# Kernel tuning notes

Measured on AMD Instinct MI355X. Metric: run time of the kernel, lower is better.

## Reference

```python
import jax, jax.numpy as jnp
import numpy as np

N_E = 100000   # codebook size (hard-coded 50000/50000 split in source)
E = 768        # e_dim
BETA = 0.25
K = 10         # top-k in source
BUF = 300000   # codebook_used buffer length
SPLIT = 768
B = 512


def _l2n(x):
    # F.normalize(p=2, dim=-1): x / max(||x||, eps)
    return x / jnp.maximum(jnp.linalg.norm(x, axis=-1, keepdims=True), 1e-12)


def _dist(x, y):
    return (x * x).sum(1, keepdims=True) + (y * y).sum(1) - 2.0 * (x @ y.T)


def _quantize(z_flat, cb_norm):
    z_norm = _l2n(z_flat)
    d = _dist(z_norm, cb_norm)
    neg_vals, idx = jax.lax.top_k(-d, K)          # smallest distances, ascending
    w = jax.nn.softmax(neg_vals, axis=1)          # softmax(-distance)
    z_q = jnp.einsum('bk,bkd->bd', w, cb_norm[idx])
    vq = jnp.mean((z_q - jax.lax.stop_gradient(z_flat)) ** 2)
    commit = BETA * jnp.mean((jax.lax.stop_gradient(z_q) - z_flat) ** 2)
    z_q_ste = z_flat + jax.lax.stop_gradient(z_q - z_flat)   # straight-through
    return z_q_ste, vq, commit, idx


def _usage(buf, idx):
    # rolling FIFO buffer of recent code indices; usage = #unique / n_e
    flat = idx.reshape(-1).astype(buf.dtype)
    L = flat.shape[0]
    buf = jnp.concatenate([buf[L:], flat])
    used = jnp.zeros((N_E,), jnp.int32).at[buf].set(1).sum() / N_E
    return buf, used


def setup_inputs() -> dict:
    key = jax.random.key(0)
    ks = jax.random.split(key, 12)
    inp = {
        'z': jax.random.normal(ks[0], (B, 2 * SPLIT), jnp.float32),
        'text_features': jax.random.normal(ks[1], (B, E), jnp.float32),
        'graph_node_features': jax.random.normal(ks[2], (B, E), jnp.float32),
        'batch': B,
        'codebook': jax.random.normal(ks[3], (N_E, E), jnp.float32),
        # MultiheadAttention value/out projections (q/k projs have no effect for seq_len=1)
        'Wv': jax.random.normal(ks[4], (E, E), jnp.float32) * 0.02,
        'bv': jnp.zeros((E,), jnp.float32),
        'Wo': jax.random.normal(ks[5], (E, E), jnp.float32) * 0.02,
        'bo': jnp.zeros((E,), jnp.float32),
        'Wpt': jax.random.normal(ks[6], (E, SPLIT), jnp.float32) * 0.02,
        'bpt': jnp.zeros((E,), jnp.float32),
        'Wpg': jax.random.normal(ks[7], (E, SPLIT), jnp.float32) * 0.02,
        'bpg': jnp.zeros((E,), jnp.float32),
        'codebook_used': jnp.zeros((BUF,), jnp.int32),
    }
    return inp


def reference(z, text_features, graph_node_features, batch, codebook,
              Wv, bv, Wo, bo, Wpt, bpt, Wpg, bpg, codebook_used):
    # --- get_shared_info ---
    # cross_attn with query/key/value all of seq_len 1: softmax over a single key
    # is exactly 1, so output == out_proj(v_proj(value)); eval mode (no dropout).
    vproj = lambda x: x @ Wv.T + bv
    oproj = lambda x: x @ Wo.T + bo
    z_flat_text = oproj(vproj(graph_node_features))   # query=text, value=graph
    z_flat_graph = oproj(vproj(text_features))         # query=graph, value=text

    cb_norm = _l2n(codebook)
    zq_t, vq_t, cm_t, idx_t = _quantize(z_flat_text, cb_norm)
    zq_g, vq_g, cm_g, idx_g = _quantize(z_flat_graph, cb_norm)
    shared_vq = vq_t + vq_g
    shared_commit = cm_t + cm_g
    buf, shared_usage = _usage(codebook_used, jnp.concatenate([idx_t, idx_g], axis=-1))

    # shared_embedding split back into text/graph halves
    shared_text_embedding, shared_graph_embedding = zq_t, zq_g

    # --- specific embeddings ---
    z_text_embedding = z[:, :SPLIT]
    z_graph_embedding = z[:, SPLIT:]
    pt = z_text_embedding @ Wpt.T + bpt
    pg = z_graph_embedding @ Wpg.T + bpg
    cb_text_norm = _l2n(codebook[:50000])
    cb_graph_norm = _l2n(codebook[-50000:])

    sq_t, svq_t, scm_t, sidx_t = _quantize(pt, cb_text_norm)
    buf, text_usage = _usage(buf, sidx_t)
    sq_g, svq_g, scm_g, sidx_g = _quantize(pg, cb_graph_norm)
    buf, graph_usage = _usage(buf, sidx_g)

    return (z_graph_embedding, z_text_embedding,
            shared_text_embedding, shared_graph_embedding,
            shared_vq, shared_commit,
            sq_t, svq_t, scm_t,
            sq_g, svq_g, scm_g,
            shared_usage, text_usage, graph_usage)
```

## Files before the change

### kernel.cpp

```cpp
#include <hip/hip_runtime.h>
#include <hip/hip_bf16.h>

typedef __attribute__((ext_vector_type(8))) short bf16x8;
typedef __attribute__((ext_vector_type(4))) short short4v;
typedef __attribute__((ext_vector_type(4))) float f32x4;

#define NE_      100000
#define EDIM     768
#define HALFCB   50000
#define CHK      1024
#define NCH      49
#define NQT      12
#define QS       1536
#define KTOP     10

#define RN_OFF   0ULL
#define Q_OFF    401408ULL
#define Y_OFF    3547136ULL
#define ZF_OFF   6692864ULL
#define PT_OFF   9838592ULL
#define PG_OFF   11411456ULL
#define CAND_OFF 12984320ULL
#define APP_OFF  25026560ULL
#define FLAG_OFF 25108480ULL
#define CNT_OFF  26308480ULL
#define ACC_OFF  26308544ULL
#define WS_NEED  26308608ULL

#define O_ZQT    786432u
#define O_ZQG    1179648u
#define O_SVQ    1572864u
#define O_SQT    1572866u
#define O_SVQT   1966082u
#define O_SQG    1966084u
#define O_SVQG   2359300u
#define O_USE    2359302u

__device__ __forceinline__ short f2bf(float f) {
  union { float f; unsigned u; } v; v.f = f;
  unsigned r = v.u + 0x7FFFu + ((v.u >> 16) & 1u);
  return (short)(r >> 16);
}

__device__ __forceinline__ void ins10(float v, int idx, float s[10], int id[10]) {
  if (v <= s[0]) return;
  #pragma unroll
  for (int j = 0; j < 10; ++j) {
    bool shift = (j < 9) && (v > s[j + 1]);
    float ns = shift ? s[j + 1] : v;
    int   ni = shift ? id[j + 1] : idx;
    bool upd = shift || (v > s[j]);
    s[j]  = upd ? ns : s[j];
    id[j] = upd ? ni : id[j];
  }
}

__global__ __launch_bounds__(256) void k_rnorm(const float* __restrict__ cb, float* __restrict__ rn) {
  int row = blockIdx.x * 4 + (threadIdx.x >> 6);
  int lane = threadIdx.x & 63;
  const float4* p = (const float4*)(cb + (size_t)row * EDIM);
  float ss = 0.f;
  #pragma unroll
  for (int j = 0; j < 3; ++j) {
    float4 v = p[j * 64 + lane];
    ss += v.x * v.x + v.y * v.y + v.z * v.z + v.w * v.w;
  }
  #pragma unroll
  for (int off = 32; off; off >>= 1) ss += __shfl_xor(ss, off);
  if (lane == 0) rn[row] = 1.0f / fmaxf(sqrtf(ss), 1e-12f);
}

__global__ __launch_bounds__(256) void k_copyz(const float* __restrict__ z, float* __restrict__ out) {
  int i = blockIdx.x * 256 + threadIdx.x;
  int r = i / 192, c = i - r * 192;
  const float4* zr = (const float4*)z + (size_t)r * 384;
  float4 t = zr[c];
  float4 g = zr[192 + c];
  ((float4*)out)[i] = g;
  ((float4*)(out + 393216))[i] = t;
}

__global__ __launch_bounds__(256, 2) void k_gemm_proj(
    const float* __restrict__ A, int lda, const float* __restrict__ W,
    const float* __restrict__ bias, float* __restrict__ C) {
  __shared__ short As[128][72];
  __shared__ short Bs[128][72];
  int tid = threadIdx.x;
  int wave = tid >> 6, lane = tid & 63;
  int wr = wave >> 1, wc = wave & 1;
  int r16 = lane & 15, g8 = (lane >> 4) * 8;
  int m0 = blockIdx.x * 128, n0 = blockIdx.y * 128;
  f32x4 acc[4][4];
  f32x4 zv = {0.f, 0.f, 0.f, 0.f};
  #pragma unroll
  for (int m = 0; m < 4; ++m)
    #pragma unroll
    for (int n = 0; n < 4; ++n) acc[m][n] = zv;

  for (int ks = 0; ks < 12; ++ks) {
    float4 av[8], wv[8];
    #pragma unroll
    for (int i = 0; i < 8; ++i) {
      int id = i * 256 + tid;
      int r = id >> 4, c4 = id & 15;
      av[i] = *((const float4*)(A + (size_t)(m0 + r) * lda + ks * 64) + c4);
      wv[i] = *((const float4*)(W + (size_t)(n0 + r) * EDIM + ks * 64) + c4);
    }
    __syncthreads();
    #pragma unroll
    for (int i = 0; i < 8; ++i) {
      int id = i * 256 + tid;
      int r = id >> 4, c4 = id & 15;
      short4v sa = { f2bf(av[i].x), f2bf(av[i].y), f2bf(av[i].z), f2bf(av[i].w) };
      short4v sw = { f2bf(wv[i].x), f2bf(wv[i].y), f2bf(wv[i].z), f2bf(wv[i].w) };
      *(short4v*)&As[r][c4 * 4] = sa;
      *(short4v*)&Bs[r][c4 * 4] = sw;
    }
    __syncthreads();
    #pragma unroll
    for (int kk = 0; kk < 64; kk += 32) {
      bf16x8 a[4], b[4];
      #pragma unroll
      for (int m = 0; m < 4; ++m) a[m] = *(const bf16x8*)&As[wr * 64 + m * 16 + r16][kk + g8];
      #pragma unroll
      for (int n = 0; n < 4; ++n) b[n] = *(const bf16x8*)&Bs[wc * 64 + n * 16 + r16][kk + g8];
      #pragma unroll
      for (int m = 0; m < 4; ++m)
        #pragma unroll
        for (int n = 0; n < 4; ++n)
          acc[m][n] = __builtin_amdgcn_mfma_f32_16x16x32_bf16(a[m], b[n], acc[m][n], 0, 0, 0);
    }
  }
  #pragma unroll
  for (int n = 0; n < 4; ++n) {
    int col = n0 + wc * 64 + n * 16 + r16;
    float bb = bias[col];
    #pragma unroll
    for (int m = 0; m < 4; ++m) {
      int row = m0 + wr * 64 + m * 16 + (lane >> 4) * 4;
      #pragma unroll
      for (int j = 0; j < 4; ++j)
        C[(size_t)(row + j) * EDIM + col] = acc[m][n][j] + bb;
    }
  }
}

__global__ __launch_bounds__(256) void k_normq(
    const float* __restrict__ ZF, const float* __restrict__ PT,
    const float* __restrict__ PG, short* __restrict__ Q) {
  int row = blockIdx.x * 4 + (threadIdx.x >> 6);
  int lane = threadIdx.x & 63;
  const float* src = (row < 1024) ? ZF + (size_t)row * EDIM
                   : (row < 1536) ? PT + (size_t)(row - 1024) * EDIM
                                  : PG + (size_t)(row - 1536) * EDIM;
  const float4* p = (const float4*)src;
  float4 v[3];
  float ss = 0.f;
  #pragma unroll
  for (int j = 0; j < 3; ++j) {
    v[j] = p[j * 64 + lane];
    ss += v[j].x * v[j].x + v[j].y * v[j].y + v[j].z * v[j].z + v[j].w * v[j].w;
  }
  #pragma unroll
  for (int off = 32; off; off >>= 1) ss += __shfl_xor(ss, off);
  float r = 1.0f / fmaxf(sqrtf(ss), 1e-12f);
  #pragma unroll
  for (int j = 0; j < 3; ++j) {
    short4v s = { f2bf(v[j].x * r), f2bf(v[j].y * r), f2bf(v[j].z * r), f2bf(v[j].w * r) };
    *(short4v*)(Q + (size_t)row * EDIM + (size_t)(j * 64 + lane) * 4) = s;
  }
}

__global__ __launch_bounds__(256, 2) void k_scores(
    const float* __restrict__ cb, const float* __restrict__ rn,
    const short* __restrict__ Q, float2* __restrict__ cand) {
  __shared__ short As[128][72];
  __shared__ short Bs[128][72];
  __shared__ float Sc[128][65];
  int qt = blockIdx.x, ck = blockIdx.y, hh = blockIdx.z;
  int tid = threadIdx.x;
  int wave = tid >> 6, lane = tid & 63;
  int wr = wave >> 1, wc = wave & 1;
  int r16 = lane & 15, g8 = (lane >> 4) * 8;
  int row0 = ck * CHK;
  int nvalid = min(CHK, HALFCB - row0);
  int grow0 = hh * HALFCB + row0;
  int hmax = hh * HALFCB + HALFCB - 1;
  int qbase = qt * 128;
  int q = tid & 127, seg = tid >> 7;

  float s10[10]; int id10[10];
  #pragma unroll
  for (int k = 0; k < 10; ++k) { s10[k] = -3.4e38f; id10[k] = 0; }

  for (int mt = 0; mt < 8; ++mt) {
    f32x4 acc[4][4];
    f32x4 zv = {0.f, 0.f, 0.f, 0.f};
    #pragma unroll
    for (int m = 0; m < 4; ++m)
      #pragma unroll
      for (int n = 0; n < 4; ++n) acc[m][n] = zv;

    for (int ks = 0; ks < 12; ++ks) {
      float4 av[8]; float rsv[8]; uint4 qv[4];
      #pragma unroll
      for (int i = 0; i < 8; ++i) {
        int id = i * 256 + tid;
        int r = id >> 4, c4 = id & 15;
        int gr = grow0 + mt * 128 + r;
        gr = min(gr, hmax);
        av[i] = *((const float4*)(cb + (size_t)gr * EDIM + ks * 64) + c4);
        rsv[i] = rn[gr];
      }
      #pragma unroll
      for (int i = 0; i < 4; ++i) {
        int id = i * 256 + tid;
        int s = id >> 3, c8 = id & 7;
        int slot = qbase + s;
        int qr = (hh && slot >= 1024) ? slot + 512 : slot;
        qv[i] = *((const uint4*)(Q + (size_t)qr * EDIM + ks * 64) + c8);
      }
      __syncthreads();
      #pragma unroll
      for (int i = 0; i < 8; ++i) {
        int id = i * 256 + tid;
        int r = id >> 4, c4 = id & 15;
        short4v sa = { f2bf(av[i].x * rsv[i]), f2bf(av[i].y * rsv[i]),
                       f2bf(av[i].z * rsv[i]), f2bf(av[i].w * rsv[i]) };
        *(short4v*)&As[r][c4 * 4] = sa;
      }
      #pragma unroll
      for (int i = 0; i < 4; ++i) {
        int id = i * 256 + tid;
        int s = id >> 3, c8 = id & 7;
        *(uint4*)&Bs[s][c8 * 8] = qv[i];
      }
      __syncthreads();
      #pragma unroll
      for (int kk = 0; kk < 64; kk += 32) {
        bf16x8 a[4], b[4];
        #pragma unroll
        for (int m = 0; m < 4; ++m) a[m] = *(const bf16x8*)&As[wr * 64 + m * 16 + r16][kk + g8];
        #pragma unroll
        for (int n = 0; n < 4; ++n) b[n] = *(const bf16x8*)&Bs[wc * 64 + n * 16 + r16][kk + g8];
        #pragma unroll
        for (int m = 0; m < 4; ++m)
          #pragma unroll
          for (int n = 0; n < 4; ++n)
            acc[m][n] = __builtin_amdgcn_mfma_f32_16x16x32_bf16(a[m], b[n], acc[m][n], 0, 0, 0);
      }
    }
    #pragma unroll
    for (int p = 0; p < 2; ++p) {
      __syncthreads();
      if (wr == p) {
        #pragma unroll
        for (int n = 0; n < 4; ++n) {
          int c = wc * 64 + n * 16 + r16;
          #pragma unroll
          for (int m = 0; m < 4; ++m) {
            int rl = m * 16 + (lane >> 4) * 4;
            #pragma unroll
            for (int j = 0; j < 4; ++j) Sc[c][rl + j] = acc[m][n][j];
          }
        }
      }
      __syncthreads();
      int rbase = mt * 128 + p * 64 + seg * 32;
      #pragma unroll 4
      for (int j = 0; j < 32; ++j) {
        int rr = rbase + j;
        float v = Sc[q][seg * 32 + j];
        if (rr < nvalid) ins10(v, grow0 + rr, s10, id10);
      }
    }
  }
  __syncthreads();
  float* scf = &Sc[0][0];
  #pragma unroll
  for (int k = 0; k < 10; ++k) {
    scf[tid * 20 + k] = s10[k];
    scf[tid * 20 + 10 + k] = __int_as_float(id10[k]);
  }
  __syncthreads();
  if (tid < 128) {
    int pb = (tid + 128) * 20;
    #pragma unroll
    for (int k = 0; k < 10; ++k) {
      float v = scf[pb + k];
      int ip = __float_as_int(scf[pb + 10 + k]);
      ins10(v, ip, s10, id10);
    }
    float2* cp = cand + ((size_t)(hh * QS + qbase + tid) * NCH + ck) * KTOP;
    #pragma unroll
    for (int k = 0; k < 10; ++k) cp[k] = make_float2(s10[k], __int_as_float(id10[k]));
  }
}

__global__ __launch_bounds__(256) void k_topk(
    const float2* __restrict__ cand, const float* __restrict__ cb,
    const float* __restrict__ rn, const float* __restrict__ ZF,
    const float* __restrict__ PT, const float* __restrict__ PG,
    float* __restrict__ out, int* __restrict__ app, float* __restrict__ accs) {
  int wave = threadIdx.x >> 6, lane = threadIdx.x & 63;
  int lq = blockIdx.x * 4 + wave;
  int g = lq >> 9, i = lq & 511;
  int slotA = (g == 0) ? i : (g == 1) ? 512 + i : 1024 + i;
  int halfA = (g == 3) ? 1 : 0;
  int n = (g <= 1) ? 980 : 490;
  const float2* baseA = cand + (size_t)(halfA * QS + slotA) * NCH * KTOP;
  const float2* baseB = cand + (size_t)(QS + slotA) * NCH * KTOP;

  float v[16]; int idv[16];
  #pragma unroll
  for (int j = 0; j < 16; ++j) {
    int c = lane + 64 * j;
    float2 e = make_float2(-3.4e38f, 0.f);
    if (c < n) e = (c < 490) ? baseA[c] : baseB[c - 490];
    v[j] = e.x; idv[j] = __float_as_int(e.y);
  }
  unsigned mask = 0xFFFFu;
  float s10[10]; int id10[10];
  #pragma unroll
  for (int r = 0; r < 10; ++r) {
    float bv = -3.4e38f; int bcb = 0x7fffffff; int bpk = 0;
    #pragma unroll
    for (int j = 0; j < 16; ++j) {
      bool alive = (mask >> j) & 1u;
      float vv = alive ? v[j] : -3.4e38f;
      bool take = (vv > bv) || (alive && vv == bv && idv[j] < bcb);
      if (take) { bv = vv; bcb = idv[j]; bpk = (lane << 5) | j; }
    }
    #pragma unroll
    for (int off = 1; off < 64; off <<= 1) {
      float ov = __shfl_xor(bv, off);
      int ocb = __shfl_xor(bcb, off);
      int opk = __shfl_xor(bpk, off);
      bool take = (ov > bv) || (ov == bv && ocb < bcb);
      if (take) { bv = ov; bcb = ocb; bpk = opk; }
    }
    s10[r] = bv; id10[r] = bcb;
    if ((bpk >> 5) == lane) mask &= ~(1u << (bpk & 31u));
  }
  float smax = s10[0];
  float w[10], wsum = 0.f, rnv[10];
  #pragma unroll
  for (int r = 0; r < 10; ++r) { w[r] = expf(2.0f * (s10[r] - smax)); wsum += w[r]; }
  float inv = 1.0f / wsum;
  #pragma unroll
  for (int r = 0; r < 10; ++r) { w[r] *= inv; rnv[r] = rn[id10[r]]; }

  const float* zrow = (g == 0) ? ZF + (size_t)i * EDIM
                    : (g == 1) ? ZF + (size_t)(512 + i) * EDIM
                    : (g == 2) ? PT + (size_t)i * EDIM
                               : PG + (size_t)i * EDIM;
  size_t obase = (size_t)((g == 0) ? O_ZQT : (g == 1) ? O_ZQG : (g == 2) ? O_SQT : O_SQG)
               + (size_t)i * EDIM;
  float vsum = 0.f;
  #pragma unroll
  for (int j = 0; j < 12; ++j) {
    int d = lane + 64 * j;
    float zq = 0.f;
    #pragma unroll
    for (int r = 0; r < 10; ++r) zq += w[r] * cb[(size_t)id10[r] * EDIM + d] * rnv[r];
    out[obase + d] = zq;
    float df = zq - zrow[d];
    vsum += df * df;
  }
  #pragma unroll
  for (int off = 32; off; off >>= 1) vsum += __shfl_xor(vsum, off);
  if (lane == 0) atomicAdd(&accs[g], vsum);
  if (lane < 10) {
    int val = id10[lane];
    if (g == 0)      app[i * 20 + lane] = val;
    else if (g == 1) app[i * 20 + 10 + lane] = val;
    else if (g == 2) app[10240 + i * 10 + lane] = val;
    else             app[15360 + i * 10 + lane] = val - 50000;
  }
}

__global__ __launch_bounds__(256) void k_scatter(
    const int* __restrict__ buf0, const int* __restrict__ app, int* __restrict__ flags) {
  int id = blockIdx.x * 256 + threadIdx.x;
  if (id >= 900000) return;
  int vvar = id / 300000;
  int j = id - vvar * 300000;
  int off = 10240 + 5120 * vvar;
  int keep = 300000 - off;
  int val = (j < keep) ? buf0[off + j] : app[j - keep];
  if (val >= 0 && val < NE_) flags[vvar * NE_ + val] = 1;
}

__global__ __launch_bounds__(256) void k_count(const int* __restrict__ flags, int* __restrict__ cnt) {
  int vvar = blockIdx.y;
  int base = blockIdx.x * 1024;
  int s = 0;
  for (int j = threadIdx.x; j < 1024; j += 256) {
    int idx = base + j;
    if (idx < NE_) s += flags[vvar * NE_ + idx];
  }
  #pragma unroll
  for (int off = 32; off; off >>= 1) s += __shfl_xor(s, off);
  __shared__ int ls[4];
  if ((threadIdx.x & 63) == 0) ls[threadIdx.x >> 6] = s;
  __syncthreads();
  if (threadIdx.x == 0) atomicAdd(&cnt[vvar], ls[0] + ls[1] + ls[2] + ls[3]);
}

__global__ void k_fin(const float* __restrict__ accs, const int* __restrict__ cnt,
                      float* __restrict__ out) {
  if (threadIdx.x == 0) {
    const float inv = 1.0f / (512.0f * 768.0f);
    float vt = accs[0] * inv, vg = accs[1] * inv;
    float vpt = accs[2] * inv, vpg = accs[3] * inv;
    out[O_SVQ]      = vt + vg;
    out[O_SVQ + 1]  = 0.25f * (vt + vg);
    out[O_SVQT]     = vpt;
    out[O_SVQT + 1] = 0.25f * vpt;
    out[O_SVQG]     = vpg;
    out[O_SVQG + 1] = 0.25f * vpg;
    out[O_USE]      = (float)cnt[0] / 100000.0f;
    out[O_USE + 1]  = (float)cnt[1] / 100000.0f;
    out[O_USE + 2]  = (float)cnt[2] / 100000.0f;
  }
}

extern "C" void kernel_launch(void* const* d_in, const int* in_sizes, int n_in,
                              void* d_out, int out_size, void* d_ws, size_t ws_size,
                              hipStream_t stream) {
  const float* z   = (const float*)d_in[0];
  const float* tf  = (const float*)d_in[1];
  const float* gf  = (const float*)d_in[2];
  const float* cb  = (const float*)d_in[4];
  const float* Wv  = (const float*)d_in[5];
  const float* bv  = (const float*)d_in[6];
  const float* Wo  = (const float*)d_in[7];
  const float* bo  = (const float*)d_in[8];
  const float* Wpt = (const float*)d_in[9];
  const float* bpt = (const float*)d_in[10];
  const float* Wpg = (const float*)d_in[11];
  const float* bpg = (const float*)d_in[12];
  const int* used  = (const int*)d_in[13];
  float* out = (float*)d_out;
  char* ws = (char*)d_ws;
  if (ws_size < WS_NEED) return;

  float* rn    = (float*)(ws + RN_OFF);
  short* Q     = (short*)(ws + Q_OFF);
  float* Y     = (float*)(ws + Y_OFF);
  float* ZF    = (float*)(ws + ZF_OFF);
  float* PT    = (float*)(ws + PT_OFF);
  float* PG    = (float*)(ws + PG_OFF);
  float2* cand = (float2*)(ws + CAND_OFF);
  int* app     = (int*)(ws + APP_OFF);
  int* flags   = (int*)(ws + FLAG_OFF);
  int* cnt     = (int*)(ws + CNT_OFF);
  float* accs  = (float*)(ws + ACC_OFF);

  hipMemsetAsync(ws + FLAG_OFF, 0, 1200128, stream);
  k_rnorm<<<25000, 256, 0, stream>>>(cb, rn);
  k_copyz<<<384, 256, 0, stream>>>(z, out);
  k_gemm_proj<<<dim3(4, 6), 256, 0, stream>>>(gf, 768, Wv, bv, Y);
  k_gemm_proj<<<dim3(4, 6), 256, 0, stream>>>(tf, 768, Wv, bv, Y + 512 * 768);
  k_gemm_proj<<<dim3(8, 6), 256, 0, stream>>>(Y, 768, Wo, bo, ZF);
  k_gemm_proj<<<dim3(4, 6), 256, 0, stream>>>(z, 1536, Wpt, bpt, PT);
  k_gemm_proj<<<dim3(4, 6), 256, 0, stream>>>(z + 768, 1536, Wpg, bpg, PG);
  k_normq<<<512, 256, 0, stream>>>(ZF, PT, PG, Q);
  k_scores<<<dim3(NQT, NCH, 2), 256, 0, stream>>>(cb, rn, Q, cand);
  k_topk<<<512, 256, 0, stream>>>(cand, cb, rn, ZF, PT, PG, out, app, accs);
  k_scatter<<<3516, 256, 0, stream>>>(used, app, flags);
  k_count<<<dim3(98, 3), 256, 0, stream>>>(flags, cnt);
  k_fin<<<1, 64, 0, stream>>>(accs, cnt, out);
}
```

Before: 1.520 ms.

## Pre-normalize codebook to bf16 per half and score from bf16 copy

Adds a conversion kernel that normalizes each codebook half once and stores it as bf16 in the workspace, along with the inverse norms. A new scores kernel reads this bf16 copy instead of re-reading fp32 rows and converting them per tile, which halves the bytes loaded from global memory. The scores kernel also uses a smaller score buffer in shared memory and sets occupancy to 3 blocks per CU. The work is split into two launches per half so the converted buffer is reused; this adds about 77 MB of workspace and an extra pass over the codebook. The old path is kept as a fallback when the workspace is too small.

```diff
diff --git a/kernel.cpp b/kernel.cpp
--- a/kernel.cpp
+++ b/kernel.cpp
@@ -26,6 +26,8 @@
 #define CNT_OFF  26308480ULL
 #define ACC_OFF  26308544ULL
 #define WS_NEED  26308608ULL
+#define CBN_OFF  26308608ULL
+#define WS_BIG   (CBN_OFF + 76800000ULL)
 
 #define O_ZQT    786432u
 #define O_ZQG    1179648u
@@ -68,6 +70,29 @@
   #pragma unroll
   for (int off = 32; off; off >>= 1) ss += __shfl_xor(ss, off);
   if (lane == 0) rn[row] = 1.0f / fmaxf(sqrtf(ss), 1e-12f);
+}
+
+__global__ __launch_bounds__(256) void k_cvt(const float* __restrict__ cb, int row0,
+                                             float* __restrict__ rn, short* __restrict__ cbn) {
+  int r = blockIdx.x * 4 + (threadIdx.x >> 6);
+  int lane = threadIdx.x & 63;
+  const float4* p = (const float4*)(cb + (size_t)(row0 + r) * EDIM);
+  float4 v[3];
+  float ss = 0.f;
+  #pragma unroll
+  for (int j = 0; j < 3; ++j) {
+    v[j] = p[j * 64 + lane];
+    ss += v[j].x * v[j].x + v[j].y * v[j].y + v[j].z * v[j].z + v[j].w * v[j].w;
+  }
+  #pragma unroll
+  for (int off = 32; off; off >>= 1) ss += __shfl_xor(ss, off);
+  float s = 1.0f / fmaxf(sqrtf(ss), 1e-12f);
+  if (lane == 0) rn[row0 + r] = s;
+  #pragma unroll
+  for (int j = 0; j < 3; ++j) {
+    short4v o = { f2bf(v[j].x * s), f2bf(v[j].y * s), f2bf(v[j].z * s), f2bf(v[j].w * s) };
+    *(short4v*)(cbn + (size_t)r * EDIM + (size_t)(j * 64 + lane) * 4) = o;
+  }
 }
 
 __global__ __launch_bounds__(256) void k_copyz(const float* __restrict__ z, float* __restrict__ out) {
@@ -168,6 +193,120 @@
   for (int j = 0; j < 3; ++j) {
     short4v s = { f2bf(v[j].x * r), f2bf(v[j].y * r), f2bf(v[j].z * r), f2bf(v[j].w * r) };
     *(short4v*)(Q + (size_t)row * EDIM + (size_t)(j * 64 + lane) * 4) = s;
+  }
+}
+
+__global__ __launch_bounds__(256, 3) void k_scores_bf(
+    const short* __restrict__ cbn, const short* __restrict__ Q,
+    float2* __restrict__ cand, int hh) {
+  __shared__ short As[128][72];
+  __shared__ short Bs[128][72];
+  __shared__ float Sc[128][34];
+  int qt = blockIdx.x, ck = blockIdx.y;
+  int tid = threadIdx.x;
+  int wave = tid >> 6, lane = tid & 63;
+  int wr = wave >> 1, wc = wave & 1;
+  int r16 = lane & 15, g8 = (lane >> 4) * 8;
+  int row0 = ck * CHK;
+  int nvalid = min(CHK, HALFCB - row0);
+  int idg0 = hh * HALFCB + row0;
+  int hmaxl = HALFCB - 1;
+  int qbase = qt * 128;
+  int q = tid & 127, seg = tid >> 7;
+
+  float s10[10]; int id10[10];
+  #pragma unroll
+  for (int k = 0; k < 10; ++k) { s10[k] = -3.4e38f; id10[k] = 0; }
+
+  for (int mt = 0; mt < 8; ++mt) {
+    f32x4 acc[4][4];
+    f32x4 zv = {0.f, 0.f, 0.f, 0.f};
+    #pragma unroll
+    for (int m = 0; m < 4; ++m)
+      #pragma unroll
+      for (int n = 0; n < 4; ++n) acc[m][n] = zv;
+
+    for (int ks = 0; ks < 12; ++ks) {
+      uint4 av[4], qv[4];
+      #pragma unroll
+      for (int i = 0; i < 4; ++i) {
+        int id = i * 256 + tid;
+        int r = id >> 3, c8 = id & 7;
+        int gr = min(row0 + mt * 128 + r, hmaxl);
+        av[i] = *((const uint4*)(cbn + (size_t)gr * EDIM + ks * 64) + c8);
+        int slot = qbase + r;
+        int qr = (hh && slot >= 1024) ? slot + 512 : slot;
+        qv[i] = *((const uint4*)(Q + (size_t)qr * EDIM + ks * 64) + c8);
+      }
+      __syncthreads();
+      #pragma unroll
+      for (int i = 0; i < 4; ++i) {
+        int id = i * 256 + tid;
+        int r = id >> 3, c8 = id & 7;
+        *(uint4*)&As[r][c8 * 8] = av[i];
+        *(uint4*)&Bs[r][c8 * 8] = qv[i];
+      }
+      __syncthreads();
+      #pragma unroll
+      for (int kk = 0; kk < 64; kk += 32) {
+        bf16x8 a[4], b[4];
+        #pragma unroll
+        for (int m = 0; m < 4; ++m) a[m] = *(const bf16x8*)&As[wr * 64 + m * 16 + r16][kk + g8];
+        #pragma unroll
+        for (int n = 0; n < 4; ++n) b[n] = *(const bf16x8*)&Bs[wc * 64 + n * 16 + r16][kk + g8];
+        #pragma unroll
+        for (int m = 0; m < 4; ++m)
+          #pragma unroll
+          for (int n = 0; n < 4; ++n)
+            acc[m][n] = __builtin_amdgcn_mfma_f32_16x16x32_bf16(a[m], b[n], acc[m][n], 0, 0, 0);
+      }
+    }
+    #pragma unroll
+    for (int p = 0; p < 4; ++p) {
+      __syncthreads();
+      if (wr == (p >> 1)) {
+        int mbase = (p & 1) * 2;
+        #pragma unroll
+        for (int n = 0; n < 4; ++n) {
+          int c = wc * 64 + n * 16 + r16;
+          #pragma unroll
+          for (int m2 = 0; m2 < 2; ++m2) {
+            int rl = m2 * 16 + (lane >> 4) * 4;
+            #pragma unroll
+            for (int j = 0; j < 4; ++j) Sc[c][rl + j] = acc[mbase + m2][n][j];
+          }
+        }
+      }
+      __syncthreads();
+      int rbase = mt * 128 + p * 32 + seg * 16;
+      #pragma unroll
+      for (int j2 = 0; j2 < 8; ++j2) {
+        float2 vv = *(const float2*)&Sc[q][seg * 16 + j2 * 2];
+        int rr = rbase + j2 * 2;
+        if (rr < nvalid)     ins10(vv.x, idg0 + rr,     s10, id10);
+        if (rr + 1 < nvalid) ins10(vv.y, idg0 + rr + 1, s10, id10);
+      }
+    }
+  }
+  __syncthreads();
+  float* scf = (float*)&As[0][0];
+  #pragma unroll
+  for (int k = 0; k < 10; ++k) {
+    scf[tid * 20 + k] = s10[k];
+    scf[tid * 20 + 10 + k] = __int_as_float(id10[k]);
+  }
+  __syncthreads();
+  if (tid < 128) {
+    int pb = (tid + 128) * 20;
+    #pragma unroll
+    for (int k = 0; k < 10; ++k) {
+      float v = scf[pb + k];
+      int ip = __float_as_int(scf[pb + 10 + k]);
+      ins10(v, ip, s10, id10);
+    }
+    float2* cp = cand + ((size_t)(hh * QS + qbase + tid) * NCH + ck) * KTOP;
+    #pragma unroll
+    for (int k = 0; k < 10; ++k) cp[k] = make_float2(s10[k], __int_as_float(id10[k]));
   }
 }
 
@@ -456,9 +595,10 @@
   int* flags   = (int*)(ws + FLAG_OFF);
   int* cnt     = (int*)(ws + CNT_OFF);
   float* accs  = (float*)(ws + ACC_OFF);
+  short* CBN   = (short*)(ws + CBN_OFF);
+  bool big = (ws_size >= WS_BIG);
 
   hipMemsetAsync(ws + FLAG_OFF, 0, 1200128, stream);
-  k_rnorm<<<25000, 256, 0, stream>>>(cb, rn);
   k_copyz<<<384, 256, 0, stream>>>(z, out);
   k_gemm_proj<<<dim3(4, 6), 256, 0, stream>>>(gf, 768, Wv, bv, Y);
   k_gemm_proj<<<dim3(4, 6), 256, 0, stream>>>(tf, 768, Wv, bv, Y + 512 * 768);
@@ -466,7 +606,15 @@
   k_gemm_proj<<<dim3(4, 6), 256, 0, stream>>>(z, 1536, Wpt, bpt, PT);
   k_gemm_proj<<<dim3(4, 6), 256, 0, stream>>>(z + 768, 1536, Wpg, bpg, PG);
   k_normq<<<512, 256, 0, stream>>>(ZF, PT, PG, Q);
-  k_scores<<<dim3(NQT, NCH, 2), 256, 0, stream>>>(cb, rn, Q, cand);
+  if (big) {
+    for (int hh = 0; hh < 2; ++hh) {
+      k_cvt<<<12500, 256, 0, stream>>>(cb, hh * HALFCB, rn, CBN);
+      k_scores_bf<<<dim3(NQT, NCH), 256, 0, stream>>>(CBN, Q, cand, hh);
+    }
+  } else {
+    k_rnorm<<<25000, 256, 0, stream>>>(cb, rn);
+    k_scores<<<dim3(NQT, NCH, 2), 256, 0, stream>>>(cb, rn, Q, cand);
+  }
   k_topk<<<512, 256, 0, stream>>>(cand, cb, rn, ZF, PT, PG, out, app, accs);
   k_scatter<<<3516, 256, 0, stream>>>(used, app, flags);
   k_count<<<dim3(98, 3), 256, 0, stream>>>(flags, cnt);
```

Measured after the change: 2.161 ms. +42.2%, slower.

## Pre-normalize codebook to bf16 workspace and score with 64-query tiles

Applied to the files above, without the earlier changes.

Adds a conversion kernel that normalizes each codebook row and writes it as bf16 into the workspace. A new scoring kernel then reads that half-width data directly, using 64-query tiles with register double-buffered loads. This removes the per-tile fp32 load, scale and convert work from the scoring GEMM and halves the codebook bytes it streams. It adds a full extra pass over the codebook and needs a much larger workspace, so the code falls back to the old path when the workspace is too small.

```diff
diff --git a/kernel.cpp b/kernel.cpp
--- a/kernel.cpp
+++ b/kernel.cpp
@@ -10,7 +10,6 @@
 #define HALFCB   50000
 #define CHK      1024
 #define NCH      49
-#define NQT      12
 #define QS       1536
 #define KTOP     10
 
@@ -26,6 +25,9 @@
 #define CNT_OFF  26308480ULL
 #define ACC_OFF  26308544ULL
 #define WS_NEED  26308608ULL
+#define CBN_OFF  26308608ULL
+#define WS_BIG   (CBN_OFF + 76800000ULL)
+#define WS_BIG2  (CBN_OFF + 153600000ULL)
 
 #define O_ZQT    786432u
 #define O_ZQG    1179648u
@@ -68,6 +70,29 @@
   #pragma unroll
   for (int off = 32; off; off >>= 1) ss += __shfl_xor(ss, off);
   if (lane == 0) rn[row] = 1.0f / fmaxf(sqrtf(ss), 1e-12f);
+}
+
+__global__ __launch_bounds__(256) void k_cvt(const float* __restrict__ cb, int row0,
+                                             float* __restrict__ rn, short* __restrict__ cbn) {
+  int r = blockIdx.x * 4 + (threadIdx.x >> 6);
+  int lane = threadIdx.x & 63;
+  const float4* p = (const float4*)(cb + (size_t)(row0 + r) * EDIM);
+  float4 v[3];
+  float ss = 0.f;
+  #pragma unroll
+  for (int j = 0; j < 3; ++j) {
+    v[j] = p[j * 64 + lane];
+    ss += v[j].x * v[j].x + v[j].y * v[j].y + v[j].z * v[j].z + v[j].w * v[j].w;
+  }
+  #pragma unroll
+  for (int off = 32; off; off >>= 1) ss += __shfl_xor(ss, off);
+  float s = 1.0f / fmaxf(sqrtf(ss), 1e-12f);
+  if (lane == 0) rn[row0 + r] = s;
+  #pragma unroll
+  for (int j = 0; j < 3; ++j) {
+    short4v o = { f2bf(v[j].x * s), f2bf(v[j].y * s), f2bf(v[j].z * s), f2bf(v[j].w * s) };
+    *(short4v*)(cbn + (size_t)r * EDIM + (size_t)(j * 64 + lane) * 4) = o;
+  }
 }
 
 __global__ __launch_bounds__(256) void k_copyz(const float* __restrict__ z, float* __restrict__ out) {
@@ -169,6 +194,142 @@
     short4v s = { f2bf(v[j].x * r), f2bf(v[j].y * r), f2bf(v[j].z * r), f2bf(v[j].w * r) };
     *(short4v*)(Q + (size_t)row * EDIM + (size_t)(j * 64 + lane) * 4) = s;
   }
+}
+
+__global__ __launch_bounds__(256) void k_sc64(
+    const short* __restrict__ cbn, const short* __restrict__ Qp,
+    float2* __restrict__ cand, int hzArg, int zsel) {
+  __shared__ short As[128][72];
+  __shared__ short Bs[64][72];
+  int qt = blockIdx.x, ck = blockIdx.y;
+  int hz = zsel ? (int)blockIdx.z : hzArg;
+  const short* ch = cbn + (size_t)(zsel ? blockIdx.z : 0) * ((size_t)HALFCB * EDIM);
+  int tid = threadIdx.x;
+  int wave = tid >> 6, lane = tid & 63;
+  int wr = wave >> 1, wc = wave & 1;
+  int r16 = lane & 15, g8 = (lane >> 4) * 8;
+  int row0 = ck * CHK;
+  int nvalid = min(CHK, HALFCB - row0);
+  int idg0 = hz * HALFCB + row0;
+  int hmaxl = HALFCB - 1;
+  int qbase = qt * 64;
+
+  float sA[10], sB[10]; int iA[10], iB[10];
+  #pragma unroll
+  for (int k = 0; k < 10; ++k) { sA[k] = -3.4e38f; iA[k] = 0; sB[k] = -3.4e38f; iB[k] = 0; }
+
+  uint4 avA[4], qvA[2], avB[4], qvB[2];
+  f32x4 zv = {0.f, 0.f, 0.f, 0.f};
+
+#define LOADN(MT, KS, AV, QV) do { \
+    _Pragma("unroll") \
+    for (int i_ = 0; i_ < 4; ++i_) { int id_ = i_ * 256 + tid; int r_ = id_ >> 3, c8_ = id_ & 7; \
+      int gr_ = min(row0 + (MT) * 128 + r_, hmaxl); \
+      AV[i_] = *((const uint4*)(ch + (size_t)gr_ * EDIM + (KS) * 64) + c8_); } \
+    _Pragma("unroll") \
+    for (int i_ = 0; i_ < 2; ++i_) { int id_ = i_ * 256 + tid; int r_ = id_ >> 3, c8_ = id_ & 7; \
+      int slot_ = qbase + r_; int qr_ = (hz && slot_ >= 1024) ? slot_ + 512 : slot_; \
+      QV[i_] = *((const uint4*)(Qp + (size_t)qr_ * EDIM + (KS) * 64) + c8_); } \
+  } while (0)
+
+#define STOREB(AV, QV) do { \
+    _Pragma("unroll") \
+    for (int i_ = 0; i_ < 4; ++i_) { int id_ = i_ * 256 + tid; int r_ = id_ >> 3, c8_ = id_ & 7; \
+      *(uint4*)&As[r_][c8_ * 8] = AV[i_]; } \
+    _Pragma("unroll") \
+    for (int i_ = 0; i_ < 2; ++i_) { int id_ = i_ * 256 + tid; int r_ = id_ >> 3, c8_ = id_ & 7; \
+      *(uint4*)&Bs[r_][c8_ * 8] = QV[i_]; } \
+  } while (0)
+
+#define MFMAS do { \
+    _Pragma("unroll") \
+    for (int kk_ = 0; kk_ < 64; kk_ += 32) { \
+      bf16x8 a_[4], b_[2]; \
+      _Pragma("unroll") for (int m_ = 0; m_ < 4; ++m_) \
+        a_[m_] = *(const bf16x8*)&As[wr * 64 + m_ * 16 + r16][kk_ + g8]; \
+      _Pragma("unroll") for (int n_ = 0; n_ < 2; ++n_) \
+        b_[n_] = *(const bf16x8*)&Bs[wc * 32 + n_ * 16 + r16][kk_ + g8]; \
+      _Pragma("unroll") for (int m_ = 0; m_ < 4; ++m_) \
+        _Pragma("unroll") for (int n_ = 0; n_ < 2; ++n_) \
+          acc[m_][n_] = __builtin_amdgcn_mfma_f32_16x16x32_bf16(a_[m_], b_[n_], acc[m_][n_], 0, 0, 0); \
+    } \
+  } while (0)
+
+  LOADN(0, 0, avA, qvA);
+  #pragma unroll 1
+  for (int mt = 0; mt < 8; ++mt) {
+    f32x4 acc[4][2];
+    #pragma unroll
+    for (int m = 0; m < 4; ++m) { acc[m][0] = zv; acc[m][1] = zv; }
+
+    #pragma unroll
+    for (int kp = 0; kp < 6; ++kp) {
+      __syncthreads(); STOREB(avA, qvA); __syncthreads();
+      LOADN(mt, kp * 2 + 1, avB, qvB);
+      MFMAS;
+      __syncthreads(); STOREB(avB, qvB); __syncthreads();
+      if (kp < 5) { LOADN(mt, kp * 2 + 2, avA, qvA); }
+      else if (mt < 7) { LOADN(mt + 1, 0, avA, qvA); }
+      MFMAS;
+    }
+    int rbase = mt * 128 + wr * 64 + (lane >> 4) * 4;
+    #pragma unroll
+    for (int m = 0; m < 4; ++m) {
+      #pragma unroll
+      for (int j = 0; j < 4; ++j) {
+        int rr = rbase + m * 16 + j;
+        if (rr < nvalid) {
+          ins10(acc[m][0][j], idg0 + rr, sA, iA);
+          ins10(acc[m][1][j], idg0 + rr, sB, iB);
+        }
+      }
+    }
+  }
+
+  #pragma unroll
+  for (int rd = 0; rd < 2; ++rd) {
+    int off = rd ? 32 : 16;
+    float tv[10]; int ti[10];
+    #pragma unroll
+    for (int k = 0; k < 10; ++k) { tv[k] = __shfl_xor(sA[k], off); ti[k] = __shfl_xor(iA[k], off); }
+    #pragma unroll
+    for (int k = 0; k < 10; ++k) ins10(tv[k], ti[k], sA, iA);
+    #pragma unroll
+    for (int k = 0; k < 10; ++k) { tv[k] = __shfl_xor(sB[k], off); ti[k] = __shfl_xor(iB[k], off); }
+    #pragma unroll
+    for (int k = 0; k < 10; ++k) ins10(tv[k], ti[k], sB, iB);
+  }
+
+  __syncthreads();
+  float2* mbuf = (float2*)&As[0][0];
+  if (wr == 1 && (lane & 48) == 0) {
+    #pragma unroll
+    for (int k = 0; k < 10; ++k) {
+      mbuf[((wc * 2 + 0) * 16 + r16) * 10 + k] = make_float2(sA[k], __int_as_float(iA[k]));
+      mbuf[((wc * 2 + 1) * 16 + r16) * 10 + k] = make_float2(sB[k], __int_as_float(iB[k]));
+    }
+  }
+  __syncthreads();
+  if (wr == 0 && (lane & 48) == 0) {
+    #pragma unroll
+    for (int k = 0; k < 10; ++k) {
+      float2 e = mbuf[((wc * 2 + 0) * 16 + r16) * 10 + k];
+      ins10(e.x, __float_as_int(e.y), sA, iA);
+      float2 f = mbuf[((wc * 2 + 1) * 16 + r16) * 10 + k];
+      ins10(f.x, __float_as_int(f.y), sB, iB);
+    }
+    int q0 = qbase + wc * 32 + r16;
+    float2* cp0 = cand + ((size_t)(hz * QS + q0) * NCH + ck) * KTOP;
+    float2* cp1 = cand + ((size_t)(hz * QS + q0 + 16) * NCH + ck) * KTOP;
+    #pragma unroll
+    for (int k = 0; k < 10; ++k) {
+      cp0[k] = make_float2(sA[k], __int_as_float(iA[k]));
+      cp1[k] = make_float2(sB[k], __int_as_float(iB[k]));
+    }
+  }
+#undef LOADN
+#undef STOREB
+#undef MFMAS
 }
 
 __global__ __launch_bounds__(256, 2) void k_scores(
@@ -456,9 +617,11 @@
   int* flags   = (int*)(ws + FLAG_OFF);
   int* cnt     = (int*)(ws + CNT_OFF);
   float* accs  = (float*)(ws + ACC_OFF);
+  short* CBN   = (short*)(ws + CBN_OFF);
+  bool big2 = (ws_size >= WS_BIG2);
+  bool big  = (ws_size >= WS_BIG);
 
   hipMemsetAsync(ws + FLAG_OFF, 0, 1200128, stream);
-  k_rnorm<<<25000, 256, 0, stream>>>(cb, rn);
   k_copyz<<<384, 256, 0, stream>>>(z, out);
   k_gemm_proj<<<dim3(4, 6), 256, 0, stream>>>(gf, 768, Wv, bv, Y);
   k_gemm_proj<<<dim3(4, 6), 256, 0, stream>>>(tf, 768, Wv, bv, Y + 512 * 768);
@@ -466,7 +629,19 @@
   k_gemm_proj<<<dim3(4, 6), 256, 0, stream>>>(z, 1536, Wpt, bpt, PT);
   k_gemm_proj<<<dim3(4, 6), 256, 0, stream>>>(z + 768, 1536, Wpg, bpg, PG);
   k_normq<<<512, 256, 0, stream>>>(ZF, PT, PG, Q);
-  k_scores<<<dim3(NQT, NCH, 2), 256, 0, stream>>>(cb, rn, Q, cand);
+  if (big2) {
+    k_cvt<<<12500, 256, 0, stream>>>(cb, 0, rn, CBN);
+    k_cvt<<<12500, 256, 0, stream>>>(cb, HALFCB, rn, CBN + (size_t)HALFCB * EDIM);
+    k_sc64<<<dim3(24, NCH, 2), 256, 0, stream>>>(CBN, Q, cand, 0, 1);
+  } else if (big) {
+    for (int hh = 0; hh < 2; ++hh) {
+      k_cvt<<<12500, 256, 0, stream>>>(cb, hh * HALFCB, rn, CBN);
+      k_sc64<<<dim3(24, NCH, 1), 256, 0, stream>>>(CBN, Q, cand, hh, 0);
+    }
+  } else {
+    k_rnorm<<<25000, 256, 0, stream>>>(cb, rn);
+    k_scores<<<dim3(12, NCH, 2), 256, 0, stream>>>(cb, rn, Q, cand);
+  }
   k_topk<<<512, 256, 0, stream>>>(cand, cb, rn, ZF, PT, PG, out, app, accs);
   k_scatter<<<3516, 256, 0, stream>>>(used, app, flags);
   k_count<<<dim3(98, 3), 256, 0, stream>>>(flags, cnt);
```

New measurement: 2.545 ms. 67.5% more time.
